# Kernel optimization log

Hardware: AMD Instinct MI355X
Metric: run time of the kernel (lower is better)

The kernel has to match this reference:

```python
import jax, jax.numpy as jnp
import numpy as np

N = 20000      # nodes
C = 64         # in_channels
E = 640000     # edges (avg degree 32)
B = 8          # graphs in batch
STEPS = 16     # 2**4 diffusion steps per cascade
FENG = np.array([4, 8, 9, 12, 13, 14])  # feng_filters()


def make_wavelet():
    # Fixed 4x17 wavelet constructor: Psi_j = P^{2^{j-1}} - P^{2^j}
    W = jnp.zeros((4, 17), dtype=jnp.float32)
    W = W.at[0, 1].set(-1.0).at[0, 2].set(1.0)
    W = W.at[1, 2].set(-1.0).at[1, 4].set(1.0)
    W = W.at[2, 4].set(-1.0).at[2, 8].set(1.0)
    W = W.at[3, 8].set(-1.0).at[3, 16].set(1.0)
    return W


def setup_inputs() -> dict:
    key = jax.random.key(0)
    k1, k2, k3 = jax.random.split(key, 3)
    x = jax.random.normal(k1, (N, C), dtype=jnp.float32)
    edge_index = jax.random.randint(k2, (2, E), 0, N, dtype=jnp.int32)
    batch = jnp.sort(jax.random.randint(k3, (N,), 0, B, dtype=jnp.int32))
    wavelet_constructor = make_wavelet()
    return {"x": x, "edge_index": edge_index, "batch": batch,
            "wavelet_constructor": wavelet_constructor}


def _gcn_norm(edge_index, n, dtype):
    # Add self loops; norm = d^-1/2[row] * d^-1/2[col] (gcn_norm, weight 1)
    row, col = edge_index
    loop = jnp.arange(n, dtype=row.dtype)
    row = jnp.concatenate([row, loop])
    col = jnp.concatenate([col, loop])
    deg = jax.ops.segment_sum(jnp.ones_like(row, dtype=dtype), col, num_segments=n)
    dinv = jnp.where(deg > 0, jax.lax.rsqrt(deg), 0.0)
    return row, col, dinv[row] * dinv[col]


def _cascade(h0, row, col, norm, n):
    # 16 lazy-random-walk diffusion steps: h <- 0.5*(h + A_hat h); keep all levels.
    nb = norm.reshape((-1,) + (1,) * (h0.ndim - 1))
    def step(h, _):
        msg = jax.ops.segment_sum(h[row] * nb, col, num_segments=n)
        h = 0.5 * (h + msg)
        return h, h
    _, ys = jax.lax.scan(step, h0, None, length=STEPS)
    return jnp.concatenate([h0[None], ys], axis=0)  # [17, ...]


def reference(x, edge_index, batch, wavelet_constructor):
    n = x.shape[0]
    row, col, norm = _gcn_norm(edge_index, n, x.dtype)

    # First-order scattering
    S0 = x[:, :, None]                                       # [N, C, 1]
    lev1 = _cascade(S0, row, col, norm, n)                   # [17, N, C, 1]
    sub1 = jnp.einsum('wl,lnck->wnck', wavelet_constructor, lev1)[..., 0]  # [4, N, C]
    S1 = jnp.abs(jnp.transpose(sub1, (1, 2, 0)))             # [N, C, 4]

    # Second-order scattering
    lev2 = _cascade(S1, row, col, norm, n)                   # [17, N, C, 4]
    sub2 = jnp.einsum('wl,lncb->wncb', wavelet_constructor, lev2)          # [4, N, C, 4]
    S2_swapped = jnp.abs(jnp.transpose(sub2, (1, 0, 3, 2))).reshape(n, 16, -1)  # [N, 16, C]
    S2 = S2_swapped[:, FENG]                                 # [N, 6, C]

    feats = jnp.concatenate(
        [jnp.transpose(jnp.concatenate([S0, S1], axis=2), (0, 2, 1)), S2], axis=1)  # [N, 11, C]

    # Statistical-moments aggregation per graph
    d = feats.reshape(n, -1)                                 # [N, 11*C]
    cnt = jnp.maximum(jax.ops.segment_sum(jnp.ones((n,), d.dtype), batch,
                                          num_segments=B), 1.0)[:, None]
    mean = jax.ops.segment_sum(d, batch, num_segments=B) / cnt
    dev = d - mean[batch]
    var = jax.ops.segment_sum(dev ** 2, batch, num_segments=B) / cnt
    m3 = jax.ops.segment_sum(dev ** 3, batch, num_segments=B) / cnt
    m4 = jax.ops.segment_sum(dev ** 4, batch, num_segments=B) / cnt
    safe = var > 0
    vsafe = jnp.where(safe, var, 1.0)
    skew = jnp.where(safe, m3 / vsafe ** 1.5, 0.0)   # NaN (zero-var) -> 0
    kurt = jnp.where(safe, m4 / vsafe ** 2, -3.0)    # NaN (zero-var) -> -3
    out = jnp.concatenate([mean, var, skew, kurt], axis=1)   # [B, 4*11*C]
    return out, wavelet_constructor
```

## Files before the change

kernel.cpp:

```cpp
#include <hip/hip_runtime.h>
#include <hip/hip_fp16.h>

#define NB 8
#define CAP 128
#define NFEAT 704
#define MSLICE 8
#define PSLICE (MSLICE * 4)


__global__ void count_edges(const int* __restrict__ ei, int E, int* __restrict__ cnt) {
    int e = blockIdx.x * blockDim.x + threadIdx.x;
    if (e < E) atomicAdd(&cnt[ei[E + e]], 1);
}

__global__ void compute_dinv(const int* __restrict__ cnt, float* __restrict__ dinv, int n) {
    int v = blockIdx.x * blockDim.x + threadIdx.x;
    if (v < n) dinv[v] = rsqrtf((float)(cnt[v] + 1));
}

__global__ void fill_edges(const int* __restrict__ ei, int E, const float* __restrict__ dinv,
                           int* __restrict__ cursor, unsigned int* __restrict__ pairs) {
    int e = blockIdx.x * blockDim.x + threadIdx.x;
    if (e < E) {
        int r = ei[e], c = ei[E + e];
        int pos = atomicAdd(&cursor[c], 1);
        if (pos < CAP) {
            float w = dinv[r] * dinv[c];
            __half hw = __float2half_rn(w);
            unsigned short hb = *reinterpret_cast<unsigned short*>(&hw);
            pairs[(size_t)c * CAP + pos] = (unsigned int)(r & 0xFFFF) | ((unsigned int)hb << 16);
        }
    }
}

__global__ void pad_edges(const int* __restrict__ cnt, unsigned int* __restrict__ pairs, int n) {
    int v = blockIdx.x * blockDim.x + threadIdx.x;
    if (v >= n) return;
    int c = min(cnt[v], CAP);
    int c4 = (c + 3) & ~3;
    for (int j = c; j < c4; ++j) pairs[(size_t)v * CAP + j] = 0u;
}

__global__ void batch_bounds(const int* __restrict__ batch, int n, int* __restrict__ boff) {
    int i = blockIdx.x * blockDim.x + threadIdx.x;
    if (i >= n) return;
    int b = batch[i];
    int pb = (i == 0) ? -1 : batch[i - 1];
    for (int k = pb + 1; k <= b; ++k) boff[k] = i;
    if (i == n - 1) {
        for (int k = b + 1; k <= NB; ++k) boff[k] = n;
    }
}

__global__ void convert_f16(const float* __restrict__ x, unsigned short* __restrict__ xh, int n) {
    int i = blockIdx.x * blockDim.x + threadIdx.x;
    if (i < n) {
        __half h = __float2half_rn(x[i]);
        xh[i] = *reinterpret_cast<unsigned short*>(&h);
    }
}


__device__ __forceinline__ float h2f16(unsigned short h) {
    __half hh = *reinterpret_cast<__half*>(&h);
    return __half2float(hh);
}

__device__ __forceinline__ void fma_h4(float w, uint2 m, float* a) {
    float2 f0 = __half22float2(*reinterpret_cast<__half2*>(&m.x));
    float2 f1 = __half22float2(*reinterpret_cast<__half2*>(&m.y));
    a[0] += w * f0.x; a[1] += w * f0.y; a[2] += w * f1.x; a[3] += w * f1.y;
}

template <int NU>
__global__ __launch_bounds__(256) void cascade_k(
    const float* __restrict__ selfp, int sstride, long usz,
    const unsigned short* __restrict__ mirp, long musz,
    float* __restrict__ state_out, unsigned short* __restrict__ mir_out,
    const unsigned int* __restrict__ pairs, const int* __restrict__ cnt,
    const float* __restrict__ dinv, int n,
    int s,
    float* __restrict__ prevb,
    float* __restrict__ S1, unsigned short* __restrict__ S1h,
    float* __restrict__ S2)
{
    int lane = threadIdx.x & 63, widx = threadIdx.x >> 6;
    int node = blockIdx.x * 4 + widx;
    if (node >= n) return;
    node = __builtin_amdgcn_readfirstlane(node);

    int deg = min(cnt[node], CAP);
    int deg4 = (deg + 3) & ~3;
    float dv = dinv[node];
    float selfw = 1.f + dv * dv;

    int sub = lane >> 4;
    int cg  = lane & 15;

    const unsigned int* pb = pairs + (size_t)node * CAP;

    float a[NU][4];
#pragma unroll
    for (int u = 0; u < NU; ++u)
#pragma unroll
        for (int k = 0; k < 4; ++k) a[u][k] = 0.f;

    int j = 0;
    for (; j + 8 <= deg4; j += 8) {
        uint4 qA = *reinterpret_cast<const uint4*>(pb + j);
        uint4 qB = *reinterpret_cast<const uint4*>(pb + j + 4);
        unsigned int eA = sub < 2 ? (sub == 0 ? qA.x : qA.y) : (sub == 2 ? qA.z : qA.w);
        unsigned int eB = sub < 2 ? (sub == 0 ? qB.x : qB.y) : (sub == 2 ? qB.z : qB.w);
        int   sA = (int)(eA & 0xFFFFu);
        float wA = h2f16((unsigned short)(eA >> 16));
        int   sB = (int)(eB & 0xFFFFu);
        float wB = h2f16((unsigned short)(eB >> 16));
        uint2 gA[NU], gB[NU];
#pragma unroll
        for (int u = 0; u < NU; ++u)
            gA[u] = *reinterpret_cast<const uint2*>(mirp + (size_t)u * musz + (size_t)sA * 64 + cg * 4);
#pragma unroll
        for (int u = 0; u < NU; ++u)
            gB[u] = *reinterpret_cast<const uint2*>(mirp + (size_t)u * musz + (size_t)sB * 64 + cg * 4);
#pragma unroll
        for (int u = 0; u < NU; ++u) {
            fma_h4(wA, gA[u], a[u]);
            fma_h4(wB, gB[u], a[u]);
        }
    }
    if (j < deg4) {
        uint4 qA = *reinterpret_cast<const uint4*>(pb + j);
        unsigned int eA = sub < 2 ? (sub == 0 ? qA.x : qA.y) : (sub == 2 ? qA.z : qA.w);
        int   sA = (int)(eA & 0xFFFFu);
        float wA = h2f16((unsigned short)(eA >> 16));
        uint2 gA[NU];
#pragma unroll
        for (int u = 0; u < NU; ++u)
            gA[u] = *reinterpret_cast<const uint2*>(mirp + (size_t)u * musz + (size_t)sA * 64 + cg * 4);
#pragma unroll
        for (int u = 0; u < NU; ++u) fma_h4(wA, gA[u], a[u]);
    }

#pragma unroll
    for (int m = 16; m <= 32; m <<= 1) {
#pragma unroll
        for (int u = 0; u < NU; ++u) {
#pragma unroll
            for (int k = 0; k < 4; ++k) a[u][k] += __shfl_xor(a[u][k], m, 64);
        }
    }

    if (lane < 16) {
#pragma unroll
        for (int u = 0; u < NU; ++u) {
            const float* srow = selfp + (size_t)u * usz + (size_t)node * sstride + cg * 4;
            float4 hv = *reinterpret_cast<const float4*>(srow);
            float4 v;
            v.x = 0.5f * (selfw * hv.x + a[u][0]);
            v.y = 0.5f * (selfw * hv.y + a[u][1]);
            v.z = 0.5f * (selfw * hv.z + a[u][2]);
            v.w = 0.5f * (selfw * hv.w + a[u][3]);
            size_t oidx = (size_t)u * n * 64 + (size_t)node * 64 + cg * 4;
            *reinterpret_cast<float4*>(state_out + oidx) = v;
            __half2 p01 = __float22half2_rn(make_float2(v.x, v.y));
            __half2 p23 = __float22half2_rn(make_float2(v.z, v.w));
            uint2 mo;
            mo.x = *reinterpret_cast<unsigned int*>(&p01);
            mo.y = *reinterpret_cast<unsigned int*>(&p23);
            *reinterpret_cast<uint2*>(mir_out + oidx) = mo;

            int snap = (NU == 1) ? 1 : (2 << u);
            float* prow = prevb + oidx;
            if (s == snap) {
                *reinterpret_cast<float4*>(prow) = v;
            } else if (s > snap && (s == 2 || s == 4 || s == 8 || s == 16)) {
                float4 pv = *reinterpret_cast<const float4*>(prow);
                *reinterpret_cast<float4*>(prow) = v;
                float4 d;
                d.x = fabsf(v.x - pv.x); d.y = fabsf(v.y - pv.y);
                d.z = fabsf(v.z - pv.z); d.w = fabsf(v.w - pv.w);
                if (NU == 1) {
                    int slot = (s == 2) ? 0 : (s == 4) ? 1 : (s == 8) ? 2 : 3;
                    *reinterpret_cast<float4*>(S1 + (size_t)node * 256 + slot * 64 + cg * 4) = d;
                    if (slot < 3) {
                        __half2 d01 = __float22half2_rn(make_float2(d.x, d.y));
                        __half2 d23 = __float22half2_rn(make_float2(d.z, d.w));
                        uint2 dh;
                        dh.x = *reinterpret_cast<unsigned int*>(&d01);
                        dh.y = *reinterpret_cast<unsigned int*>(&d23);
                        *reinterpret_cast<uint2*>(S1h + (size_t)slot * n * 64 + (size_t)node * 64 + cg * 4) = dh;
                    }
                } else {
                    int slt;
                    if (u == 0)      slt = (s == 4) ? 0 : (s == 8) ? 1 : 3;
                    else if (u == 1) slt = (s == 8) ? 2 : 4;
                    else             slt = 5;
                    *reinterpret_cast<float4*>(S2 + (size_t)node * 384 + slt * 64 + cg * 4) = d;
                }
            }
        }
    }
}


__global__ __launch_bounds__(256) void moments_part(
    const float* __restrict__ x, const float* __restrict__ S1,
    const float* __restrict__ S2, const int* __restrict__ boff,
    double* __restrict__ part)
{
    int bid = blockIdx.x;
    int slice = bid % MSLICE;
    int k = (bid / MSLICE) % 11;
    int b = bid / (11 * MSLICE);
    int c = threadIdx.x & 63, sub = threadIdx.x >> 6;

    const float* base; int stride;
    if (k == 0)      { base = x  + c;                stride = 64;  }
    else if (k <= 4) { base = S1 + (k - 1) * 64 + c; stride = 256; }
    else             { base = S2 + (k - 5) * 64 + c; stride = 384; }

    int s0 = boff[b], s1e = boff[b + 1];
    int cntb = s1e - s0;
    int per = (cntb + MSLICE - 1) / MSLICE;
    int i0 = s0 + slice * per;
    int i1 = min(s1e, i0 + per);

    double a1 = 0, a2 = 0, a3 = 0, a4 = 0;
    for (int i = i0 + sub; i < i1; i += 4) {
        double v = (double)base[(size_t)i * stride];
        double qq = v * v;
        a1 += v; a2 += qq; a3 += qq * v; a4 += qq * qq;
    }
    int f = k * 64 + c;
    double* qp = part + ((((size_t)slice * 4 + sub) * NB + b) * NFEAT + f) * 4;
    qp[0] = a1; qp[1] = a2; qp[2] = a3; qp[3] = a4;
}

__global__ void finalize_k(const double* __restrict__ part, const int* __restrict__ boff,
                           const float* __restrict__ W, float* __restrict__ out) {
    int i = blockIdx.x * blockDim.x + threadIdx.x;
    if (i < NB * NFEAT) {
        int b = i / NFEAT, f = i % NFEAT;
        double s1 = 0, s2 = 0, s3 = 0, s4 = 0;
        for (int s = 0; s < PSLICE; ++s) {
            const double* qp = part + (((size_t)s * NB + b) * NFEAT + f) * 4;
            s1 += qp[0]; s2 += qp[1]; s3 += qp[2]; s4 += qp[3];
        }
        double cn = (double)max(boff[b + 1] - boff[b], 1);
        double mean = s1 / cn;
        double e2 = s2 / cn, e3 = s3 / cn, e4 = s4 / cn;
        double var = e2 - mean * mean;
        double m3 = e3 - 3.0 * mean * e2 + 2.0 * mean * mean * mean;
        double m4 = e4 - 4.0 * mean * e3 + 6.0 * mean * mean * e2 - 3.0 * mean * mean * mean * mean;
        float skew, kurt;
        if (var > 0.0) {
            double vs = var * sqrt(var);
            skew = (float)(m3 / vs);
            kurt = (float)(m4 / (var * var));
        } else {
            skew = 0.f; kurt = -3.f;
        }
        out[b * 2816 + f]        = (float)mean;
        out[b * 2816 + 704 + f]  = (float)var;
        out[b * 2816 + 1408 + f] = skew;
        out[b * 2816 + 2112 + f] = kurt;
    } else if (i < NB * NFEAT + 68) {
        int j = i - NB * NFEAT;
        out[NB * 2816 + j] = W[j];
    }
}


extern "C" void kernel_launch(void* const* d_in, const int* in_sizes, int n_in,
                              void* d_out, int out_size, void* d_ws, size_t ws_size,
                              hipStream_t stream) {
    const float* x     = (const float*)d_in[0];
    const int*   ei    = (const int*)d_in[1];
    const int*   batch = (const int*)d_in[2];
    const float* W     = (const float*)d_in[3];
    int N = in_sizes[0] / 64;
    int E = in_sizes[1] / 2;
    float* out = (float*)d_out;

    char* p = (char*)d_ws;
    auto alloc = [&](size_t bytes) { char* r = p; p += (bytes + 255) & ~255ULL; return r; };
    float* dinv  = (float*)alloc((size_t)N * 4);
    int*   cnt   = (int*)alloc((size_t)N * 4);
    int*   cursor= (int*)alloc((size_t)N * 4);
    int*   boff  = (int*)alloc((NB + 1) * 4);
    double* part = (double*)alloc((size_t)PSLICE * NB * NFEAT * 4 * 8);
    unsigned int* pairs = (unsigned int*)alloc((size_t)N * CAP * 4);
    float* S1    = (float*)alloc((size_t)N * 256 * 4);
    float* S2    = (float*)alloc((size_t)N * 384 * 4);
    unsigned short* S1h = (unsigned short*)alloc((size_t)3 * N * 64 * 2);
    unsigned short* xh  = (unsigned short*)alloc((size_t)N * 64 * 2);
    float* bufA  = (float*)alloc((size_t)3 * N * 64 * 4);
    float* bufB  = (float*)alloc((size_t)3 * N * 64 * 4);
    float* prev  = (float*)alloc((size_t)3 * N * 64 * 4);
    unsigned short* mirA = (unsigned short*)alloc((size_t)3 * N * 64 * 2);
    unsigned short* mirB = (unsigned short*)alloc((size_t)3 * N * 64 * 2);

    hipMemsetAsync(cnt, 0, (size_t)N * 4, stream);
    hipMemsetAsync(cursor, 0, (size_t)N * 4, stream);

    count_edges<<<(E + 255) / 256, 256, 0, stream>>>(ei, E, cnt);
    compute_dinv<<<(N + 255) / 256, 256, 0, stream>>>(cnt, dinv, N);
    fill_edges<<<(E + 255) / 256, 256, 0, stream>>>(ei, E, dinv, cursor, pairs);
    pad_edges<<<(N + 255) / 256, 256, 0, stream>>>(cnt, pairs, N);
    batch_bounds<<<(N + 255) / 256, 256, 0, stream>>>(batch, N, boff);
    convert_f16<<<(N * 64 + 255) / 256, 256, 0, stream>>>(x, xh, N * 64);

    long nu = (long)N * 64;
    int cgrid = (N + 3) / 4;

    for (int s = 1; s <= 16; ++s) {
        float* so = (s & 1) ? bufA : bufB;
        unsigned short* mo = (s & 1) ? mirA : mirB;
        const float* selfp; int sstride; long usz;
        const unsigned short* mirp; long musz;
        if (s == 1) { selfp = x; sstride = 64; usz = 0; mirp = xh; musz = 0; }
        else {
            selfp = (s & 1) ? bufB : bufA; sstride = 64; usz = nu;
            mirp = (s & 1) ? mirB : mirA; musz = nu;
        }
        cascade_k<1><<<cgrid, 256, 0, stream>>>(selfp, sstride, usz, mirp, musz, so, mo,
                                                pairs, cnt, dinv, N, s, prev, S1, S1h, S2);
    }

    for (int s = 1; s <= 16; ++s) {
        float* so = (s & 1) ? bufA : bufB;
        unsigned short* mo = (s & 1) ? mirA : mirB;
        const float* selfp; int sstride; long usz;
        const unsigned short* mirp; long musz;
        if (s == 1) { selfp = S1; sstride = 256; usz = 64; mirp = S1h; musz = nu; }
        else {
            selfp = (s & 1) ? bufB : bufA; sstride = 64; usz = nu;
            mirp = (s & 1) ? mirB : mirA; musz = nu;
        }
        cascade_k<3><<<cgrid, 256, 0, stream>>>(selfp, sstride, usz, mirp, musz, so, mo,
                                                pairs, cnt, dinv, N, s, prev, S1, S1h, S2);
    }

    moments_part<<<NB * 11 * MSLICE, 256, 0, stream>>>(x, S1, S2, boff, part);

    int fin_threads = NB * NFEAT + 68;
    finalize_k<<<(fin_threads + 255) / 256, 256, 0, stream>>>(part, boff, W, out);
}
```

Baseline: 939.9 us.

## Overlap first- and second-order cascades in shared diffusion kernels and prefetch edge lists

The second-order cascade only needs S1 slots 0-2, which are ready after step 8 of the first-order cascade. The change starts the second-order cascade at that point and runs it in the same kernel launches as first-order steps 9-16, so each launch reads the edge list once for both cascades. This cuts the launch count from 32 to 24 and gives each wave more independent gathers. The edge-pair loop is also software-pipelined: the next 8 pair entries are prefetched, and padding is widened to multiples of 8 to remove the tail branch. The cost is higher register pressure from four accumulator sets and separate buffers for each cascade.

```diff
diff --git a/kernel.cpp b/kernel.cpp
--- a/kernel.cpp
+++ b/kernel.cpp
@@ -37,8 +37,8 @@
     int v = blockIdx.x * blockDim.x + threadIdx.x;
     if (v >= n) return;
     int c = min(cnt[v], CAP);
-    int c4 = (c + 3) & ~3;
-    for (int j = c; j < c4; ++j) pairs[(size_t)v * CAP + j] = 0u;
+    int c8 = (c + 7) & ~7;
+    for (int j = c; j < c8; ++j) pairs[(size_t)v * CAP + j] = 0u;
 }
 
 __global__ void batch_bounds(const int* __restrict__ batch, int n, int* __restrict__ boff) {
@@ -72,15 +72,26 @@
     a[0] += w * f0.x; a[1] += w * f0.y; a[2] += w * f1.x; a[3] += w * f1.y;
 }
 
-template <int NU>
+__device__ __forceinline__ uint2 pack_h4(float4 v) {
+    __half2 p01 = __float22half2_rn(make_float2(v.x, v.y));
+    __half2 p23 = __float22half2_rn(make_float2(v.z, v.w));
+    uint2 r;
+    r.x = *reinterpret_cast<unsigned int*>(&p01);
+    r.y = *reinterpret_cast<unsigned int*>(&p23);
+    return r;
+}
+
+template <int U1, int U2>
 __global__ __launch_bounds__(256) void cascade_k(
-    const float* __restrict__ selfp, int sstride, long usz,
-    const unsigned short* __restrict__ mirp, long musz,
-    float* __restrict__ state_out, unsigned short* __restrict__ mir_out,
+    const float* __restrict__ self1, const unsigned short* __restrict__ mir1,
+    float* __restrict__ state1o, unsigned short* __restrict__ mir1o,
+    float* __restrict__ prev1, int s1,
+    const float* __restrict__ self2, int sstride2, long usz2,
+    const unsigned short* __restrict__ mir2, long musz2,
+    float* __restrict__ state2o, unsigned short* __restrict__ mir2o,
+    float* __restrict__ prev2, int s2,
     const unsigned int* __restrict__ pairs, const int* __restrict__ cnt,
     const float* __restrict__ dinv, int n,
-    int s,
-    float* __restrict__ prevb,
     float* __restrict__ S1, unsigned short* __restrict__ S1h,
     float* __restrict__ S2)
 {
@@ -90,7 +101,7 @@
     node = __builtin_amdgcn_readfirstlane(node);
 
     int deg = min(cnt[node], CAP);
-    int deg4 = (deg + 3) & ~3;
+    int deg8 = (deg + 7) & ~7;
     float dv = dinv[node];
     float selfw = 1.f + dv * dv;
 
@@ -99,104 +110,121 @@
 
     const unsigned int* pb = pairs + (size_t)node * CAP;
 
-    float a[NU][4];
-#pragma unroll
-    for (int u = 0; u < NU; ++u)
-#pragma unroll
-        for (int k = 0; k < 4; ++k) a[u][k] = 0.f;
-
-    int j = 0;
-    for (; j + 8 <= deg4; j += 8) {
-        uint4 qA = *reinterpret_cast<const uint4*>(pb + j);
-        uint4 qB = *reinterpret_cast<const uint4*>(pb + j + 4);
-        unsigned int eA = sub < 2 ? (sub == 0 ? qA.x : qA.y) : (sub == 2 ? qA.z : qA.w);
-        unsigned int eB = sub < 2 ? (sub == 0 ? qB.x : qB.y) : (sub == 2 ? qB.z : qB.w);
-        int   sA = (int)(eA & 0xFFFFu);
-        float wA = h2f16((unsigned short)(eA >> 16));
-        int   sB = (int)(eB & 0xFFFFu);
-        float wB = h2f16((unsigned short)(eB >> 16));
-        uint2 gA[NU], gB[NU];
-#pragma unroll
-        for (int u = 0; u < NU; ++u)
-            gA[u] = *reinterpret_cast<const uint2*>(mirp + (size_t)u * musz + (size_t)sA * 64 + cg * 4);
-#pragma unroll
-        for (int u = 0; u < NU; ++u)
-            gB[u] = *reinterpret_cast<const uint2*>(mirp + (size_t)u * musz + (size_t)sB * 64 + cg * 4);
-#pragma unroll
-        for (int u = 0; u < NU; ++u) {
-            fma_h4(wA, gA[u], a[u]);
-            fma_h4(wB, gB[u], a[u]);
-        }
-    }
-    if (j < deg4) {
-        uint4 qA = *reinterpret_cast<const uint4*>(pb + j);
-        unsigned int eA = sub < 2 ? (sub == 0 ? qA.x : qA.y) : (sub == 2 ? qA.z : qA.w);
-        int   sA = (int)(eA & 0xFFFFu);
-        float wA = h2f16((unsigned short)(eA >> 16));
-        uint2 gA[NU];
-#pragma unroll
-        for (int u = 0; u < NU; ++u)
-            gA[u] = *reinterpret_cast<const uint2*>(mirp + (size_t)u * musz + (size_t)sA * 64 + cg * 4);
-#pragma unroll
-        for (int u = 0; u < NU; ++u) fma_h4(wA, gA[u], a[u]);
+    float a1[U1 ? U1 : 1][4], a2[U2 ? U2 : 1][4];
+#pragma unroll
+    for (int u = 0; u < (U1 ? U1 : 1); ++u)
+#pragma unroll
+        for (int k = 0; k < 4; ++k) a1[u][k] = 0.f;
+#pragma unroll
+    for (int u = 0; u < (U2 ? U2 : 1); ++u)
+#pragma unroll
+        for (int k = 0; k < 4; ++k) a2[u][k] = 0.f;
+
+    if (deg8 > 0) {
+        uint4 qA = *reinterpret_cast<const uint4*>(pb);
+        uint4 qB = *reinterpret_cast<const uint4*>(pb + 4);
+        int j = 0;
+        while (true) {
+            int jn = j + 8;
+            bool more = jn < deg8;
+            uint4 nA, nB;
+            if (more) {
+                nA = *reinterpret_cast<const uint4*>(pb + jn);
+                nB = *reinterpret_cast<const uint4*>(pb + jn + 4);
+            }
+            unsigned int eA = sub < 2 ? (sub == 0 ? qA.x : qA.y) : (sub == 2 ? qA.z : qA.w);
+            unsigned int eB = sub < 2 ? (sub == 0 ? qB.x : qB.y) : (sub == 2 ? qB.z : qB.w);
+            int   sA = (int)(eA & 0xFFFFu);
+            float wA = h2f16((unsigned short)(eA >> 16));
+            int   sB = (int)(eB & 0xFFFFu);
+            float wB = h2f16((unsigned short)(eB >> 16));
+            uint2 g1A, g1B, g2A[U2 ? U2 : 1], g2B[U2 ? U2 : 1];
+            if (U1) {
+                g1A = *reinterpret_cast<const uint2*>(mir1 + (size_t)sA * 64 + cg * 4);
+                g1B = *reinterpret_cast<const uint2*>(mir1 + (size_t)sB * 64 + cg * 4);
+            }
+#pragma unroll
+            for (int u = 0; u < U2; ++u)
+                g2A[u] = *reinterpret_cast<const uint2*>(mir2 + (size_t)u * musz2 + (size_t)sA * 64 + cg * 4);
+#pragma unroll
+            for (int u = 0; u < U2; ++u)
+                g2B[u] = *reinterpret_cast<const uint2*>(mir2 + (size_t)u * musz2 + (size_t)sB * 64 + cg * 4);
+            if (U1) { fma_h4(wA, g1A, a1[0]); fma_h4(wB, g1B, a1[0]); }
+#pragma unroll
+            for (int u = 0; u < U2; ++u) {
+                fma_h4(wA, g2A[u], a2[u]);
+                fma_h4(wB, g2B[u], a2[u]);
+            }
+            if (!more) break;
+            qA = nA; qB = nB; j = jn;
+        }
     }
 
 #pragma unroll
     for (int m = 16; m <= 32; m <<= 1) {
 #pragma unroll
-        for (int u = 0; u < NU; ++u) {
-#pragma unroll
-            for (int k = 0; k < 4; ++k) a[u][k] += __shfl_xor(a[u][k], m, 64);
-        }
+        for (int u = 0; u < U1; ++u)
+#pragma unroll
+            for (int k = 0; k < 4; ++k) a1[u][k] += __shfl_xor(a1[u][k], m, 64);
+#pragma unroll
+        for (int u = 0; u < U2; ++u)
+#pragma unroll
+            for (int k = 0; k < 4; ++k) a2[u][k] += __shfl_xor(a2[u][k], m, 64);
     }
 
     if (lane < 16) {
-#pragma unroll
-        for (int u = 0; u < NU; ++u) {
-            const float* srow = selfp + (size_t)u * usz + (size_t)node * sstride + cg * 4;
-            float4 hv = *reinterpret_cast<const float4*>(srow);
+        if (U1) {
+            float4 hv = *reinterpret_cast<const float4*>(self1 + (size_t)node * 64 + cg * 4);
             float4 v;
-            v.x = 0.5f * (selfw * hv.x + a[u][0]);
-            v.y = 0.5f * (selfw * hv.y + a[u][1]);
-            v.z = 0.5f * (selfw * hv.z + a[u][2]);
-            v.w = 0.5f * (selfw * hv.w + a[u][3]);
-            size_t oidx = (size_t)u * n * 64 + (size_t)node * 64 + cg * 4;
-            *reinterpret_cast<float4*>(state_out + oidx) = v;
-            __half2 p01 = __float22half2_rn(make_float2(v.x, v.y));
-            __half2 p23 = __float22half2_rn(make_float2(v.z, v.w));
-            uint2 mo;
-            mo.x = *reinterpret_cast<unsigned int*>(&p01);
-            mo.y = *reinterpret_cast<unsigned int*>(&p23);
-            *reinterpret_cast<uint2*>(mir_out + oidx) = mo;
-
-            int snap = (NU == 1) ? 1 : (2 << u);
-            float* prow = prevb + oidx;
-            if (s == snap) {
+            v.x = 0.5f * (selfw * hv.x + a1[0][0]);
+            v.y = 0.5f * (selfw * hv.y + a1[0][1]);
+            v.z = 0.5f * (selfw * hv.z + a1[0][2]);
+            v.w = 0.5f * (selfw * hv.w + a1[0][3]);
+            size_t oidx = (size_t)node * 64 + cg * 4;
+            *reinterpret_cast<float4*>(state1o + oidx) = v;
+            *reinterpret_cast<uint2*>(mir1o + oidx) = pack_h4(v);
+            float* prow = prev1 + oidx;
+            if (s1 == 1) {
                 *reinterpret_cast<float4*>(prow) = v;
-            } else if (s > snap && (s == 2 || s == 4 || s == 8 || s == 16)) {
+            } else if (s1 == 2 || s1 == 4 || s1 == 8 || s1 == 16) {
                 float4 pv = *reinterpret_cast<const float4*>(prow);
                 *reinterpret_cast<float4*>(prow) = v;
                 float4 d;
                 d.x = fabsf(v.x - pv.x); d.y = fabsf(v.y - pv.y);
                 d.z = fabsf(v.z - pv.z); d.w = fabsf(v.w - pv.w);
-                if (NU == 1) {
-                    int slot = (s == 2) ? 0 : (s == 4) ? 1 : (s == 8) ? 2 : 3;
-                    *reinterpret_cast<float4*>(S1 + (size_t)node * 256 + slot * 64 + cg * 4) = d;
-                    if (slot < 3) {
-                        __half2 d01 = __float22half2_rn(make_float2(d.x, d.y));
-                        __half2 d23 = __float22half2_rn(make_float2(d.z, d.w));
-                        uint2 dh;
-                        dh.x = *reinterpret_cast<unsigned int*>(&d01);
-                        dh.y = *reinterpret_cast<unsigned int*>(&d23);
-                        *reinterpret_cast<uint2*>(S1h + (size_t)slot * n * 64 + (size_t)node * 64 + cg * 4) = dh;
-                    }
-                } else {
-                    int slt;
-                    if (u == 0)      slt = (s == 4) ? 0 : (s == 8) ? 1 : 3;
-                    else if (u == 1) slt = (s == 8) ? 2 : 4;
-                    else             slt = 5;
-                    *reinterpret_cast<float4*>(S2 + (size_t)node * 384 + slt * 64 + cg * 4) = d;
-                }
+                int slot = (s1 == 2) ? 0 : (s1 == 4) ? 1 : (s1 == 8) ? 2 : 3;
+                *reinterpret_cast<float4*>(S1 + (size_t)node * 256 + slot * 64 + cg * 4) = d;
+                if (slot < 3)
+                    *reinterpret_cast<uint2*>(S1h + (size_t)slot * n * 64 + oidx) = pack_h4(d);
+            }
+        }
+#pragma unroll
+        for (int u = 0; u < U2; ++u) {
+            const float* srow = self2 + (size_t)u * usz2 + (size_t)node * sstride2 + cg * 4;
+            float4 hv = *reinterpret_cast<const float4*>(srow);
+            float4 v;
+            v.x = 0.5f * (selfw * hv.x + a2[u][0]);
+            v.y = 0.5f * (selfw * hv.y + a2[u][1]);
+            v.z = 0.5f * (selfw * hv.z + a2[u][2]);
+            v.w = 0.5f * (selfw * hv.w + a2[u][3]);
+            size_t oidx = (size_t)u * n * 64 + (size_t)node * 64 + cg * 4;
+            *reinterpret_cast<float4*>(state2o + oidx) = v;
+            *reinterpret_cast<uint2*>(mir2o + oidx) = pack_h4(v);
+            int snap = 2 << u;
+            float* prow = prev2 + oidx;
+            if (s2 == snap) {
+                *reinterpret_cast<float4*>(prow) = v;
+            } else if (s2 > snap && (s2 == 4 || s2 == 8 || s2 == 16)) {
+                float4 pv = *reinterpret_cast<const float4*>(prow);
+                *reinterpret_cast<float4*>(prow) = v;
+                float4 d;
+                d.x = fabsf(v.x - pv.x); d.y = fabsf(v.y - pv.y);
+                d.z = fabsf(v.z - pv.z); d.w = fabsf(v.w - pv.w);
+                int slt;
+                if (u == 0)      slt = (s2 == 4) ? 0 : (s2 == 8) ? 1 : 3;
+                else if (u == 1) slt = (s2 == 8) ? 2 : 4;
+                else             slt = 5;
+                *reinterpret_cast<float4*>(S2 + (size_t)node * 384 + slt * 64 + cg * 4) = d;
             }
         }
     }
@@ -294,11 +322,16 @@
     float* S2    = (float*)alloc((size_t)N * 384 * 4);
     unsigned short* S1h = (unsigned short*)alloc((size_t)3 * N * 64 * 2);
     unsigned short* xh  = (unsigned short*)alloc((size_t)N * 64 * 2);
-    float* bufA  = (float*)alloc((size_t)3 * N * 64 * 4);
-    float* bufB  = (float*)alloc((size_t)3 * N * 64 * 4);
-    float* prev  = (float*)alloc((size_t)3 * N * 64 * 4);
-    unsigned short* mirA = (unsigned short*)alloc((size_t)3 * N * 64 * 2);
-    unsigned short* mirB = (unsigned short*)alloc((size_t)3 * N * 64 * 2);
+    float* b1A   = (float*)alloc((size_t)N * 64 * 4);
+    float* b1B   = (float*)alloc((size_t)N * 64 * 4);
+    unsigned short* h1A = (unsigned short*)alloc((size_t)N * 64 * 2);
+    unsigned short* h1B = (unsigned short*)alloc((size_t)N * 64 * 2);
+    float* prev1 = (float*)alloc((size_t)N * 64 * 4);
+    float* b2A   = (float*)alloc((size_t)3 * N * 64 * 4);
+    float* b2B   = (float*)alloc((size_t)3 * N * 64 * 4);
+    unsigned short* h2A = (unsigned short*)alloc((size_t)3 * N * 64 * 2);
+    unsigned short* h2B = (unsigned short*)alloc((size_t)3 * N * 64 * 2);
+    float* prev2 = (float*)alloc((size_t)3 * N * 64 * 4);
 
     hipMemsetAsync(cnt, 0, (size_t)N * 4, stream);
     hipMemsetAsync(cursor, 0, (size_t)N * 4, stream);
@@ -313,32 +346,47 @@
     long nu = (long)N * 64;
     int cgrid = (N + 3) / 4;
 
-    for (int s = 1; s <= 16; ++s) {
-        float* so = (s & 1) ? bufA : bufB;
-        unsigned short* mo = (s & 1) ? mirA : mirB;
-        const float* selfp; int sstride; long usz;
-        const unsigned short* mirp; long musz;
-        if (s == 1) { selfp = x; sstride = 64; usz = 0; mirp = xh; musz = 0; }
+    for (int s = 1; s <= 8; ++s) {
+        const float* si = (s == 1) ? x  : ((s & 1) ? b1B : b1A);
+        const unsigned short* mi = (s == 1) ? xh : ((s & 1) ? h1B : h1A);
+        float* so = (s & 1) ? b1A : b1B;
+        unsigned short* mo = (s & 1) ? h1A : h1B;
+        cascade_k<1, 0><<<cgrid, 256, 0, stream>>>(
+            si, mi, so, mo, prev1, s,
+            nullptr, 0, 0, nullptr, 0, nullptr, nullptr, nullptr, 0,
+            pairs, cnt, dinv, N, S1, S1h, S2);
+    }
+
+    for (int f = 1; f <= 8; ++f) {
+        int t = f + 8;
+        const float* s1i = ((t - 1) & 1) ? b1A : b1B;
+        const unsigned short* m1i = ((t - 1) & 1) ? h1A : h1B;
+        float* s1o = (t & 1) ? b1A : b1B;
+        unsigned short* m1o = (t & 1) ? h1A : h1B;
+        const float* s2i; int sstride2; long usz2;
+        const unsigned short* m2i; long musz2;
+        if (f == 1) { s2i = S1; sstride2 = 256; usz2 = 64; m2i = S1h; musz2 = nu; }
         else {
-            selfp = (s & 1) ? bufB : bufA; sstride = 64; usz = nu;
-            mirp = (s & 1) ? mirB : mirA; musz = nu;
-        }
-        cascade_k<1><<<cgrid, 256, 0, stream>>>(selfp, sstride, usz, mirp, musz, so, mo,
-                                                pairs, cnt, dinv, N, s, prev, S1, S1h, S2);
-    }
-
-    for (int s = 1; s <= 16; ++s) {
-        float* so = (s & 1) ? bufA : bufB;
-        unsigned short* mo = (s & 1) ? mirA : mirB;
-        const float* selfp; int sstride; long usz;
-        const unsigned short* mirp; long musz;
-        if (s == 1) { selfp = S1; sstride = 256; usz = 64; mirp = S1h; musz = nu; }
-        else {
-            selfp = (s & 1) ? bufB : bufA; sstride = 64; usz = nu;
-            mirp = (s & 1) ? mirB : mirA; musz = nu;
-        }
-        cascade_k<3><<<cgrid, 256, 0, stream>>>(selfp, sstride, usz, mirp, musz, so, mo,
-                                                pairs, cnt, dinv, N, s, prev, S1, S1h, S2);
+            s2i = ((f - 1) & 1) ? b2A : b2B; sstride2 = 64; usz2 = nu;
+            m2i = ((f - 1) & 1) ? h2A : h2B; musz2 = nu;
+        }
+        float* s2o = (f & 1) ? b2A : b2B;
+        unsigned short* m2o = (f & 1) ? h2A : h2B;
+        cascade_k<1, 3><<<cgrid, 256, 0, stream>>>(
+            s1i, m1i, s1o, m1o, prev1, t,
+            s2i, sstride2, usz2, m2i, musz2, s2o, m2o, prev2, f,
+            pairs, cnt, dinv, N, S1, S1h, S2);
+    }
+
+    for (int s = 9; s <= 16; ++s) {
+        const float* s2i = ((s - 1) & 1) ? b2A : b2B;
+        const unsigned short* m2i = ((s - 1) & 1) ? h2A : h2B;
+        float* s2o = (s & 1) ? b2A : b2B;
+        unsigned short* m2o = (s & 1) ? h2A : h2B;
+        cascade_k<0, 3><<<cgrid, 256, 0, stream>>>(
+            nullptr, nullptr, nullptr, nullptr, nullptr, 0,
+            s2i, 64, nu, m2i, nu, s2o, m2o, prev2, s,
+            pairs, cnt, dinv, N, S1, S1h, S2);
     }
 
     moments_part<<<NB * 11 * MSLICE, 256, 0, stream>>>(x, S1, S2, boff, part);
```

Measured after the change: 894.7 us. 4.8% less time.

## Fuse all diffusion steps into one persistent kernel with a grid barrier

Applied to the files above, without the earlier changes.

Replaces the 32 separate cascade launches with a single persistent kernel of 768 blocks that runs all 24 steps. It synchronises between steps with an atomic-counter grid barrier, and overlaps the second-order cascade with the tail of the first (steps 9-16 run both). Per-node state and previous snapshots stay in registers, so the fp32 state and prev buffers are no longer read or written in global memory. Each 16-lane group now handles one node, with two nodes per wave-slot, instead of a whole wave per node. Risks: the barrier assumes all 768 blocks are co-resident, and its timeout break could silently corrupt results. Per-edge loads are now scalar rather than uint4, and lane imbalance from maxr may reduce efficiency.

```diff
diff --git a/kernel.cpp b/kernel.cpp
--- a/kernel.cpp
+++ b/kernel.cpp
@@ -6,6 +6,8 @@
 #define NFEAT 704
 #define MSLICE 8
 #define PSLICE (MSLICE * 4)
+#define NBLK 768
+#define KS 2
 
 
 __global__ void count_edges(const int* __restrict__ ei, int E, int* __restrict__ cnt) {
@@ -33,14 +35,6 @@
     }
 }
 
-__global__ void pad_edges(const int* __restrict__ cnt, unsigned int* __restrict__ pairs, int n) {
-    int v = blockIdx.x * blockDim.x + threadIdx.x;
-    if (v >= n) return;
-    int c = min(cnt[v], CAP);
-    int c4 = (c + 3) & ~3;
-    for (int j = c; j < c4; ++j) pairs[(size_t)v * CAP + j] = 0u;
-}
-
 __global__ void batch_bounds(const int* __restrict__ batch, int n, int* __restrict__ boff) {
     int i = blockIdx.x * blockDim.x + threadIdx.x;
     if (i >= n) return;
@@ -61,143 +55,189 @@
 }
 
 
-__device__ __forceinline__ float h2f16(unsigned short h) {
+__device__ __forceinline__ float h2f(unsigned short h) {
     __half hh = *reinterpret_cast<__half*>(&h);
     return __half2float(hh);
 }
 
-__device__ __forceinline__ void fma_h4(float w, uint2 m, float* a) {
+__device__ __forceinline__ uint2 pack4(float a, float b, float c, float d) {
+    __half2 p0 = __float22half2_rn(make_float2(a, b));
+    __half2 p1 = __float22half2_rn(make_float2(c, d));
+    uint2 r;
+    r.x = *reinterpret_cast<unsigned int*>(&p0);
+    r.y = *reinterpret_cast<unsigned int*>(&p1);
+    return r;
+}
+
+__device__ __forceinline__ void fma4(float w, uint2 m, float* a) {
     float2 f0 = __half22float2(*reinterpret_cast<__half2*>(&m.x));
     float2 f1 = __half22float2(*reinterpret_cast<__half2*>(&m.y));
     a[0] += w * f0.x; a[1] += w * f0.y; a[2] += w * f1.x; a[3] += w * f1.y;
 }
 
-template <int NU>
-__global__ __launch_bounds__(256) void cascade_k(
-    const float* __restrict__ selfp, int sstride, long usz,
-    const unsigned short* __restrict__ mirp, long musz,
-    float* __restrict__ state_out, unsigned short* __restrict__ mir_out,
+__global__ __launch_bounds__(256, 3) void persist_k(
+    const float* __restrict__ x, const unsigned short* __restrict__ xh,
+    unsigned short* __restrict__ m1a, unsigned short* __restrict__ m1b,
+    unsigned short* __restrict__ s1h,
+    unsigned short* __restrict__ m2a, unsigned short* __restrict__ m2b,
+    float* __restrict__ S1, float* __restrict__ S2,
     const unsigned int* __restrict__ pairs, const int* __restrict__ cnt,
-    const float* __restrict__ dinv, int n,
-    int s,
-    float* __restrict__ prevb,
-    float* __restrict__ S1, unsigned short* __restrict__ S1h,
-    float* __restrict__ S2)
+    const float* __restrict__ dinv, int n, int* __restrict__ bar)
 {
-    int lane = threadIdx.x & 63, widx = threadIdx.x >> 6;
-    int node = blockIdx.x * 4 + widx;
-    if (node >= n) return;
-    node = __builtin_amdgcn_readfirstlane(node);
-
-    int deg = min(cnt[node], CAP);
-    int deg4 = (deg + 3) & ~3;
-    float dv = dinv[node];
-    float selfw = 1.f + dv * dv;
-
-    int sub = lane >> 4;
-    int cg  = lane & 15;
-
-    const unsigned int* pb = pairs + (size_t)node * CAP;
-
-    float a[NU][4];
-#pragma unroll
-    for (int u = 0; u < NU; ++u)
-#pragma unroll
-        for (int k = 0; k < 4; ++k) a[u][k] = 0.f;
-
-    int j = 0;
-    for (; j + 8 <= deg4; j += 8) {
-        uint4 qA = *reinterpret_cast<const uint4*>(pb + j);
-        uint4 qB = *reinterpret_cast<const uint4*>(pb + j + 4);
-        unsigned int eA = sub < 2 ? (sub == 0 ? qA.x : qA.y) : (sub == 2 ? qA.z : qA.w);
-        unsigned int eB = sub < 2 ? (sub == 0 ? qB.x : qB.y) : (sub == 2 ? qB.z : qB.w);
-        int   sA = (int)(eA & 0xFFFFu);
-        float wA = h2f16((unsigned short)(eA >> 16));
-        int   sB = (int)(eB & 0xFFFFu);
-        float wB = h2f16((unsigned short)(eB >> 16));
-        uint2 gA[NU], gB[NU];
-#pragma unroll
-        for (int u = 0; u < NU; ++u)
-            gA[u] = *reinterpret_cast<const uint2*>(mirp + (size_t)u * musz + (size_t)sA * 64 + cg * 4);
-#pragma unroll
-        for (int u = 0; u < NU; ++u)
-            gB[u] = *reinterpret_cast<const uint2*>(mirp + (size_t)u * musz + (size_t)sB * 64 + cg * 4);
-#pragma unroll
-        for (int u = 0; u < NU; ++u) {
-            fma_h4(wA, gA[u], a[u]);
-            fma_h4(wB, gB[u], a[u]);
-        }
-    }
-    if (j < deg4) {
-        uint4 qA = *reinterpret_cast<const uint4*>(pb + j);
-        unsigned int eA = sub < 2 ? (sub == 0 ? qA.x : qA.y) : (sub == 2 ? qA.z : qA.w);
-        int   sA = (int)(eA & 0xFFFFu);
-        float wA = h2f16((unsigned short)(eA >> 16));
-        uint2 gA[NU];
-#pragma unroll
-        for (int u = 0; u < NU; ++u)
-            gA[u] = *reinterpret_cast<const uint2*>(mirp + (size_t)u * musz + (size_t)sA * 64 + cg * 4);
-#pragma unroll
-        for (int u = 0; u < NU; ++u) fma_h4(wA, gA[u], a[u]);
-    }
-
-#pragma unroll
-    for (int m = 16; m <= 32; m <<= 1) {
-#pragma unroll
-        for (int u = 0; u < NU; ++u) {
-#pragma unroll
-            for (int k = 0; k < 4; ++k) a[u][k] += __shfl_xor(a[u][k], m, 64);
-        }
-    }
-
-    if (lane < 16) {
-#pragma unroll
-        for (int u = 0; u < NU; ++u) {
-            const float* srow = selfp + (size_t)u * usz + (size_t)node * sstride + cg * 4;
-            float4 hv = *reinterpret_cast<const float4*>(srow);
-            float4 v;
-            v.x = 0.5f * (selfw * hv.x + a[u][0]);
-            v.y = 0.5f * (selfw * hv.y + a[u][1]);
-            v.z = 0.5f * (selfw * hv.z + a[u][2]);
-            v.w = 0.5f * (selfw * hv.w + a[u][3]);
-            size_t oidx = (size_t)u * n * 64 + (size_t)node * 64 + cg * 4;
-            *reinterpret_cast<float4*>(state_out + oidx) = v;
-            __half2 p01 = __float22half2_rn(make_float2(v.x, v.y));
-            __half2 p23 = __float22half2_rn(make_float2(v.z, v.w));
-            uint2 mo;
-            mo.x = *reinterpret_cast<unsigned int*>(&p01);
-            mo.y = *reinterpret_cast<unsigned int*>(&p23);
-            *reinterpret_cast<uint2*>(mir_out + oidx) = mo;
-
-            int snap = (NU == 1) ? 1 : (2 << u);
-            float* prow = prevb + oidx;
-            if (s == snap) {
-                *reinterpret_cast<float4*>(prow) = v;
-            } else if (s > snap && (s == 2 || s == 4 || s == 8 || s == 16)) {
-                float4 pv = *reinterpret_cast<const float4*>(prow);
-                *reinterpret_cast<float4*>(prow) = v;
-                float4 d;
-                d.x = fabsf(v.x - pv.x); d.y = fabsf(v.y - pv.y);
-                d.z = fabsf(v.z - pv.z); d.w = fabsf(v.w - pv.w);
-                if (NU == 1) {
-                    int slot = (s == 2) ? 0 : (s == 4) ? 1 : (s == 8) ? 2 : 3;
-                    *reinterpret_cast<float4*>(S1 + (size_t)node * 256 + slot * 64 + cg * 4) = d;
-                    if (slot < 3) {
-                        __half2 d01 = __float22half2_rn(make_float2(d.x, d.y));
-                        __half2 d23 = __float22half2_rn(make_float2(d.z, d.w));
-                        uint2 dh;
-                        dh.x = *reinterpret_cast<unsigned int*>(&d01);
-                        dh.y = *reinterpret_cast<unsigned int*>(&d23);
-                        *reinterpret_cast<uint2*>(S1h + (size_t)slot * n * 64 + (size_t)node * 64 + cg * 4) = dh;
+    const int wid = blockIdx.x * 4 + (threadIdx.x >> 6);
+    const int lane = threadIdx.x & 63;
+    const int g = lane >> 4, q = lane & 15;
+    const long nu = (long)n * 64;
+
+    int node[KS]; bool valid[KS]; int degc[KS]; float selfw[KS];
+    int maxr = 0;
+#pragma unroll
+    for (int t = 0; t < KS; ++t) {
+        node[t] = (wid * KS + t) * 4 + g;
+        valid[t] = node[t] < n;
+        degc[t] = valid[t] ? min(cnt[node[t]], CAP) : 0;
+        float dv = valid[t] ? dinv[node[t]] : 0.f;
+        selfw[t] = 1.f + dv * dv;
+        maxr = max(maxr, degc[t]);
+    }
+    maxr = max(maxr, __shfl_xor(maxr, 16, 64));
+    maxr = max(maxr, __shfl_xor(maxr, 32, 64));
+
+    float st[KS][4][4], pv[KS][4][4];
+#pragma unroll
+    for (int t = 0; t < KS; ++t) {
+        if (valid[t]) {
+            float4 xv = *reinterpret_cast<const float4*>(x + (size_t)node[t] * 64 + q * 4);
+            st[t][0][0] = xv.x; st[t][0][1] = xv.y; st[t][0][2] = xv.z; st[t][0][3] = xv.w;
+        }
+    }
+
+    for (int step = 1; step <= 24; ++step) {
+        int f = step - 8;
+        bool u1 = step <= 16;
+        bool u2 = step >= 9;
+        const unsigned short* m1r = (step == 1) ? xh : ((step & 1) ? m1b : m1a);
+        unsigned short* m1w = (step & 1) ? m1a : m1b;
+        const unsigned short* m2r = (f == 1) ? s1h : ((f & 1) ? m2b : m2a);
+        unsigned short* m2w = (f & 1) ? m2a : m2b;
+
+        float ac[KS][4][4];
+#pragma unroll
+        for (int t = 0; t < KS; ++t)
+#pragma unroll
+            for (int u = 0; u < 4; ++u)
+#pragma unroll
+                for (int k = 0; k < 4; ++k) ac[t][u][k] = 0.f;
+
+#pragma unroll 2
+        for (int j = 0; j < maxr; ++j) {
+            unsigned int e[KS];
+            int src[KS]; float w[KS];
+#pragma unroll
+            for (int t = 0; t < KS; ++t) {
+                e[t] = (j < degc[t]) ? pairs[(size_t)node[t] * CAP + j] : 0u;
+                src[t] = (int)(e[t] & 0xFFFFu);
+                w[t] = h2f((unsigned short)(e[t] >> 16));
+            }
+            uint2 g1[KS], g2[KS][3];
+            if (u1) {
+#pragma unroll
+                for (int t = 0; t < KS; ++t)
+                    g1[t] = *reinterpret_cast<const uint2*>(m1r + (size_t)src[t] * 64 + q * 4);
+            }
+            if (u2) {
+#pragma unroll
+                for (int t = 0; t < KS; ++t)
+#pragma unroll
+                    for (int u = 0; u < 3; ++u)
+                        g2[t][u] = *reinterpret_cast<const uint2*>(m2r + u * nu + (size_t)src[t] * 64 + q * 4);
+            }
+            if (u1) {
+#pragma unroll
+                for (int t = 0; t < KS; ++t) fma4(w[t], g1[t], ac[t][0]);
+            }
+            if (u2) {
+#pragma unroll
+                for (int t = 0; t < KS; ++t)
+#pragma unroll
+                    for (int u = 0; u < 3; ++u) fma4(w[t], g2[t][u], ac[t][1 + u]);
+            }
+        }
+
+#pragma unroll
+        for (int t = 0; t < KS; ++t) {
+            if (!valid[t]) continue;
+            size_t rowo = (size_t)node[t] * 64 + q * 4;
+            if (u1) {
+                float v0 = 0.5f * (selfw[t] * st[t][0][0] + ac[t][0][0]);
+                float v1 = 0.5f * (selfw[t] * st[t][0][1] + ac[t][0][1]);
+                float v2 = 0.5f * (selfw[t] * st[t][0][2] + ac[t][0][2]);
+                float v3 = 0.5f * (selfw[t] * st[t][0][3] + ac[t][0][3]);
+                st[t][0][0] = v0; st[t][0][1] = v1; st[t][0][2] = v2; st[t][0][3] = v3;
+                *reinterpret_cast<uint2*>(m1w + rowo) = pack4(v0, v1, v2, v3);
+                if (step == 1) {
+                    pv[t][0][0] = v0; pv[t][0][1] = v1; pv[t][0][2] = v2; pv[t][0][3] = v3;
+                } else if (step == 2 || step == 4 || step == 8 || step == 16) {
+                    float d0 = fabsf(v0 - pv[t][0][0]), d1 = fabsf(v1 - pv[t][0][1]);
+                    float d2 = fabsf(v2 - pv[t][0][2]), d3 = fabsf(v3 - pv[t][0][3]);
+                    pv[t][0][0] = v0; pv[t][0][1] = v1; pv[t][0][2] = v2; pv[t][0][3] = v3;
+                    int slot = (step == 2) ? 0 : (step == 4) ? 1 : (step == 8) ? 2 : 3;
+                    *reinterpret_cast<float4*>(S1 + (size_t)node[t] * 256 + slot * 64 + q * 4) =
+                        make_float4(d0, d1, d2, d3);
+                    if (step == 2) {
+                        *reinterpret_cast<uint2*>(s1h + 0 * nu + rowo) = pack4(d0, d1, d2, d3);
+                        st[t][1][0] = d0; st[t][1][1] = d1; st[t][1][2] = d2; st[t][1][3] = d3;
+                    } else if (step == 4) {
+                        *reinterpret_cast<uint2*>(s1h + 1 * nu + rowo) = pack4(d0, d1, d2, d3);
+                        st[t][2][0] = d0; st[t][2][1] = d1; st[t][2][2] = d2; st[t][2][3] = d3;
+                    } else if (step == 8) {
+                        *reinterpret_cast<uint2*>(s1h + 2 * nu + rowo) = pack4(d0, d1, d2, d3);
+                        st[t][3][0] = d0; st[t][3][1] = d1; st[t][3][2] = d2; st[t][3][3] = d3;
                     }
-                } else {
-                    int slt;
-                    if (u == 0)      slt = (s == 4) ? 0 : (s == 8) ? 1 : 3;
-                    else if (u == 1) slt = (s == 8) ? 2 : 4;
-                    else             slt = 5;
-                    *reinterpret_cast<float4*>(S2 + (size_t)node * 384 + slt * 64 + cg * 4) = d;
                 }
             }
+            if (u2) {
+#pragma unroll
+                for (int u = 0; u < 3; ++u) {
+                    float v0 = 0.5f * (selfw[t] * st[t][1 + u][0] + ac[t][1 + u][0]);
+                    float v1 = 0.5f * (selfw[t] * st[t][1 + u][1] + ac[t][1 + u][1]);
+                    float v2 = 0.5f * (selfw[t] * st[t][1 + u][2] + ac[t][1 + u][2]);
+                    float v3 = 0.5f * (selfw[t] * st[t][1 + u][3] + ac[t][1 + u][3]);
+                    st[t][1 + u][0] = v0; st[t][1 + u][1] = v1;
+                    st[t][1 + u][2] = v2; st[t][1 + u][3] = v3;
+                    *reinterpret_cast<uint2*>(m2w + u * nu + rowo) = pack4(v0, v1, v2, v3);
+                    int snap = 2 << u;
+                    if (f == snap) {
+                        pv[t][1 + u][0] = v0; pv[t][1 + u][1] = v1;
+                        pv[t][1 + u][2] = v2; pv[t][1 + u][3] = v3;
+                    } else if (f > snap && (f == 4 || f == 8 || f == 16)) {
+                        float d0 = fabsf(v0 - pv[t][1 + u][0]), d1 = fabsf(v1 - pv[t][1 + u][1]);
+                        float d2 = fabsf(v2 - pv[t][1 + u][2]), d3 = fabsf(v3 - pv[t][1 + u][3]);
+                        pv[t][1 + u][0] = v0; pv[t][1 + u][1] = v1;
+                        pv[t][1 + u][2] = v2; pv[t][1 + u][3] = v3;
+                        int slt = (u == 0) ? ((f == 4) ? 0 : (f == 8) ? 1 : 3)
+                                : (u == 1) ? ((f == 8) ? 2 : 4) : 5;
+                        *reinterpret_cast<float4*>(S2 + (size_t)node[t] * 384 + slt * 64 + q * 4) =
+                            make_float4(d0, d1, d2, d3);
+                    }
+                }
+            }
+        }
+
+        if (step < 24) {
+            __syncthreads();
+            if (threadIdx.x == 0) {
+                __threadfence();
+                atomicAdd(bar, 1);
+                int target = NBLK * step;
+                int it = 0;
+                while (atomicAdd(bar, 0) < target) {
+                    __builtin_amdgcn_s_sleep(16);
+                    if (++it > 4000000) break;
+                }
+                __threadfence();
+            }
+            __syncthreads();
         }
     }
 }
@@ -231,8 +271,8 @@
         double qq = v * v;
         a1 += v; a2 += qq; a3 += qq * v; a4 += qq * qq;
     }
-    int f = k * 64 + c;
-    double* qp = part + ((((size_t)slice * 4 + sub) * NB + b) * NFEAT + f) * 4;
+    int fi = k * 64 + c;
+    double* qp = part + ((((size_t)slice * 4 + sub) * NB + b) * NFEAT + fi) * 4;
     qp[0] = a1; qp[1] = a2; qp[2] = a3; qp[3] = a4;
 }
 
@@ -240,10 +280,10 @@
                            const float* __restrict__ W, float* __restrict__ out) {
     int i = blockIdx.x * blockDim.x + threadIdx.x;
     if (i < NB * NFEAT) {
-        int b = i / NFEAT, f = i % NFEAT;
+        int b = i / NFEAT, fi = i % NFEAT;
         double s1 = 0, s2 = 0, s3 = 0, s4 = 0;
         for (int s = 0; s < PSLICE; ++s) {
-            const double* qp = part + (((size_t)s * NB + b) * NFEAT + f) * 4;
+            const double* qp = part + (((size_t)s * NB + b) * NFEAT + fi) * 4;
             s1 += qp[0]; s2 += qp[1]; s3 += qp[2]; s4 += qp[3];
         }
         double cn = (double)max(boff[b + 1] - boff[b], 1);
@@ -260,10 +300,10 @@
         } else {
             skew = 0.f; kurt = -3.f;
         }
-        out[b * 2816 + f]        = (float)mean;
-        out[b * 2816 + 704 + f]  = (float)var;
-        out[b * 2816 + 1408 + f] = skew;
-        out[b * 2816 + 2112 + f] = kurt;
+        out[b * 2816 + fi]        = (float)mean;
+        out[b * 2816 + 704 + fi]  = (float)var;
+        out[b * 2816 + 1408 + fi] = skew;
+        out[b * 2816 + 2112 + fi] = kurt;
     } else if (i < NB * NFEAT + 68) {
         int j = i - NB * NFEAT;
         out[NB * 2816 + j] = W[j];
@@ -288,58 +328,31 @@
     int*   cnt   = (int*)alloc((size_t)N * 4);
     int*   cursor= (int*)alloc((size_t)N * 4);
     int*   boff  = (int*)alloc((NB + 1) * 4);
+    int*   bar   = (int*)alloc(256);
     double* part = (double*)alloc((size_t)PSLICE * NB * NFEAT * 4 * 8);
     unsigned int* pairs = (unsigned int*)alloc((size_t)N * CAP * 4);
     float* S1    = (float*)alloc((size_t)N * 256 * 4);
     float* S2    = (float*)alloc((size_t)N * 384 * 4);
-    unsigned short* S1h = (unsigned short*)alloc((size_t)3 * N * 64 * 2);
-    unsigned short* xh  = (unsigned short*)alloc((size_t)N * 64 * 2);
-    float* bufA  = (float*)alloc((size_t)3 * N * 64 * 4);
-    float* bufB  = (float*)alloc((size_t)3 * N * 64 * 4);
-    float* prev  = (float*)alloc((size_t)3 * N * 64 * 4);
-    unsigned short* mirA = (unsigned short*)alloc((size_t)3 * N * 64 * 2);
-    unsigned short* mirB = (unsigned short*)alloc((size_t)3 * N * 64 * 2);
+    long nu = (long)N * 64;
+    unsigned short* xh  = (unsigned short*)alloc((size_t)nu * 2);
+    unsigned short* m1a = (unsigned short*)alloc((size_t)nu * 2);
+    unsigned short* m1b = (unsigned short*)alloc((size_t)nu * 2);
+    unsigned short* s1h = (unsigned short*)alloc((size_t)3 * nu * 2);
+    unsigned short* m2a = (unsigned short*)alloc((size_t)3 * nu * 2);
+    unsigned short* m2b = (unsigned short*)alloc((size_t)3 * nu * 2);
 
     hipMemsetAsync(cnt, 0, (size_t)N * 4, stream);
     hipMemsetAsync(cursor, 0, (size_t)N * 4, stream);
+    hipMemsetAsync(bar, 0, 256, stream);
 
     count_edges<<<(E + 255) / 256, 256, 0, stream>>>(ei, E, cnt);
     compute_dinv<<<(N + 255) / 256, 256, 0, stream>>>(cnt, dinv, N);
     fill_edges<<<(E + 255) / 256, 256, 0, stream>>>(ei, E, dinv, cursor, pairs);
-    pad_edges<<<(N + 255) / 256, 256, 0, stream>>>(cnt, pairs, N);
     batch_bounds<<<(N + 255) / 256, 256, 0, stream>>>(batch, N, boff);
-    convert_f16<<<(N * 64 + 255) / 256, 256, 0, stream>>>(x, xh, N * 64);
-
-    long nu = (long)N * 64;
-    int cgrid = (N + 3) / 4;
-
-    for (int s = 1; s <= 16; ++s) {
-        float* so = (s & 1) ? bufA : bufB;
-        unsigned short* mo = (s & 1) ? mirA : mirB;
-        const float* selfp; int sstride; long usz;
-        const unsigned short* mirp; long musz;
-        if (s == 1) { selfp = x; sstride = 64; usz = 0; mirp = xh; musz = 0; }
-        else {
-            selfp = (s & 1) ? bufB : bufA; sstride = 64; usz = nu;
-            mirp = (s & 1) ? mirB : mirA; musz = nu;
-        }
-        cascade_k<1><<<cgrid, 256, 0, stream>>>(selfp, sstride, usz, mirp, musz, so, mo,
-                                                pairs, cnt, dinv, N, s, prev, S1, S1h, S2);
-    }
-
-    for (int s = 1; s <= 16; ++s) {
-        float* so = (s & 1) ? bufA : bufB;
-        unsigned short* mo = (s & 1) ? mirA : mirB;
-        const float* selfp; int sstride; long usz;
-        const unsigned short* mirp; long musz;
-        if (s == 1) { selfp = S1; sstride = 256; usz = 64; mirp = S1h; musz = nu; }
-        else {
-            selfp = (s & 1) ? bufB : bufA; sstride = 64; usz = nu;
-            mirp = (s & 1) ? mirB : mirA; musz = nu;
-        }
-        cascade_k<3><<<cgrid, 256, 0, stream>>>(selfp, sstride, usz, mirp, musz, so, mo,
-                                                pairs, cnt, dinv, N, s, prev, S1, S1h, S2);
-    }
+    convert_f16<<<((int)nu + 255) / 256, 256, 0, stream>>>(x, xh, (int)nu);
+
+    persist_k<<<NBLK, 256, 0, stream>>>(x, xh, m1a, m1b, s1h, m2a, m2b,
+                                        S1, S2, pairs, cnt, dinv, N, bar);
 
     moments_part<<<NB * 11 * MSLICE, 256, 0, stream>>>(x, S1, S2, boff, part);
 
```

Result: slower. 3.311 ms (+252.2%).
